# Kernel tuning notes

Hardware: AMD Instinct MI355X
Metric: run time of the kernel (lower is better)

Reference implementation:

```python
import jax, jax.numpy as jnp
import numpy as np

N = 50000
E = 800000
IN_DIM = 128
HID = 64
OUT_DIM = 128
NEG_SLOPE = 0.2  # PyG GATConv default


def _add_self_loops(src, dst, edge_attr, n):
    # PyG GATConv(add_self_loops=True) with edge_dim uses fill_value='mean':
    # self-loop edge_attr = mean of edge_attr of incoming edges per node.
    deg = jax.ops.segment_sum(jnp.ones((src.shape[0],), edge_attr.dtype), dst, num_segments=n)
    loop_attr = jax.ops.segment_sum(edge_attr, dst, num_segments=n) / jnp.maximum(deg, 1.0)[:, None]
    loop = jnp.arange(n, dtype=src.dtype)
    return (jnp.concatenate([src, loop]), jnp.concatenate([dst, loop]),
            jnp.concatenate([edge_attr, loop_attr], axis=0))


def _gat_conv(x, src, dst, edge_attr, W, We, a_src, a_dst, a_edge, bias, heads, out_dim, concat, n):
    src, dst, edge_attr = _add_self_loops(src, dst, edge_attr, n)
    h = (x @ W).reshape(n, heads, out_dim)                      # [N,H,D]
    he = (edge_attr @ We).reshape(-1, heads, out_dim)           # [E',H,D]
    alpha_src = jnp.einsum('nhd,hd->nh', h, a_src)
    alpha_dst = jnp.einsum('nhd,hd->nh', h, a_dst)
    alpha_edge = jnp.einsum('ehd,hd->eh', he, a_edge)
    alpha = jax.nn.leaky_relu(alpha_src[src] + alpha_dst[dst] + alpha_edge, NEG_SLOPE)  # [E',H]
    # segment softmax over edges grouped by destination node
    amax = jax.ops.segment_max(alpha, dst, num_segments=n)
    amax = jnp.where(jnp.isfinite(amax), amax, 0.0)
    ex = jnp.exp(alpha - amax[dst])
    denom = jax.ops.segment_sum(ex, dst, num_segments=n)
    coef = ex / (denom[dst] + 1e-16)                            # [E',H]
    msg = h[src] * coef[:, :, None]                             # [E',H,D]
    out = jax.ops.segment_sum(msg, dst, num_segments=n)         # [N,H,D]
    out = out.reshape(n, heads * out_dim) if concat else out.mean(axis=1)
    return out + bias


def setup_inputs() -> dict:
    key = jax.random.key(0)
    ks = jax.random.split(key, 16)
    s = 0.05
    inp = {
        'x': jax.random.normal(ks[0], (N, IN_DIM), jnp.float32),
        'edge_index': jax.random.randint(ks[1], (2, E), 0, N, dtype=jnp.int64),
        'edge_attr': jax.random.normal(ks[2], (E, 2), jnp.float32),
        # gat1: heads=4, concat -> out 4*HID
        'W1': jax.random.normal(ks[3], (IN_DIM, 4 * HID), jnp.float32) * s,
        'We1': jax.random.normal(ks[4], (2, 4 * HID), jnp.float32) * s,
        'asrc1': jax.random.normal(ks[5], (4, HID), jnp.float32) * s,
        'adst1': jax.random.normal(ks[6], (4, HID), jnp.float32) * s,
        'aedge1': jax.random.normal(ks[7], (4, HID), jnp.float32) * s,
        'b1': jnp.zeros((4 * HID,), jnp.float32),
        # gat2: heads=1, concat=False -> out OUT_DIM
        'W2': jax.random.normal(ks[8], (4 * HID, OUT_DIM), jnp.float32) * s,
        'We2': jax.random.normal(ks[9], (2, OUT_DIM), jnp.float32) * s,
        'asrc2': jax.random.normal(ks[10], (1, OUT_DIM), jnp.float32) * s,
        'adst2': jax.random.normal(ks[11], (1, OUT_DIM), jnp.float32) * s,
        'aedge2': jax.random.normal(ks[12], (1, OUT_DIM), jnp.float32) * s,
        'b2': jnp.zeros((OUT_DIM,), jnp.float32),
    }
    return inp


def reference(x, edge_index, edge_attr, W1, We1, asrc1, adst1, aedge1, b1,
              W2, We2, asrc2, adst2, aedge2, b2):
    src, dst = edge_index[0], edge_index[1]
    # dropout layers are identity in eval mode
    h = _gat_conv(x, src, dst, edge_attr, W1, We1, asrc1, adst1, aedge1, b1,
                  heads=4, out_dim=HID, concat=True, n=x.shape[0])
    h = jax.nn.elu(h)
    out = _gat_conv(h, src, dst, edge_attr, W2, We2, asrc2, adst2, aedge2, b2,
                    heads=1, out_dim=OUT_DIM, concat=False, n=x.shape[0])
    return out
```

## Files before the change

### kernel.cpp

```cpp
#include <hip/hip_runtime.h>
#include <hip/hip_bf16.h>

#define NN 50000
#define EE 800000
#define EP (EE + NN)
#define SCAN_B 2048
#define NB ((NN + SCAN_B - 1) / SCAN_B)


typedef short bf16x8 __attribute__((ext_vector_type(8)));
typedef float f32x4  __attribute__((ext_vector_type(4)));

__device__ __forceinline__ float bf2f(unsigned short u) {
    return __uint_as_float(((unsigned)u) << 16);
}
__device__ __forceinline__ unsigned short f2bf(float f) {
    unsigned b = __float_as_uint(f);
    b += 0x7fffu + ((b >> 16) & 1u);
    return (unsigned short)(b >> 16);
}

__global__ void k_prep(const float* __restrict__ We1, const float* __restrict__ ae1,
                       const float* __restrict__ We2, const float* __restrict__ ae2,
                       float* __restrict__ v,
                       const float* __restrict__ W1, unsigned short* __restrict__ W1t,
                       const float* __restrict__ W2, unsigned short* __restrict__ W2t,
                       const int* __restrict__ ei, int* __restrict__ idg,
                       const float* __restrict__ x, unsigned short* __restrict__ xb) {
    int bid = blockIdx.x, t = threadIdx.x;
    if (bid == 0) {
        if (t < 8) {
            int c = t >> 2, h = t & 3;
            float s = 0.f;
            for (int d = 0; d < 64; d++) s += We1[c * 256 + h * 64 + d] * ae1[h * 64 + d];
            v[c * 4 + h] = s;
        } else if (t < 10) {
            int c = t - 8;
            float s = 0.f;
            for (int d = 0; d < 128; d++) s += We2[c * 128 + d] * ae2[d];
            v[8 + c] = s;
        }
    } else if (bid <= 256) {
        int idx = (bid - 1) * 256 + t;
        if (idx < 32768) {
            int k = idx >> 8, n = idx & 255;
            W1t[n * 128 + k] = f2bf(W1[idx]);
        } else {
            int i = idx - 32768;
            int k = i >> 7, n = i & 127;
            W2t[n * 256 + k] = f2bf(W2[i]);
        }
    } else if (bid <= 256 + 3125) {
        int e = (bid - 257) * 256 + t;
        if (e < EE) atomicAdd(&idg[ei[EE + e]], 1);
    } else {
        int i = (bid - 3382) * 256 + t;
        if (i < NN * 128 / 4) {
            float4 vv = ((const float4*)x)[i];
            ushort4 o;
            o.x = f2bf(vv.x); o.y = f2bf(vv.y); o.z = f2bf(vv.z); o.w = f2bf(vv.w);
            ((ushort4*)xb)[i] = o;
        }
    }
}

__global__ void k_scan1(const int* __restrict__ idg, int* __restrict__ rowptr,
                        int* __restrict__ bsum) {
    __shared__ int sh[512];
    int t = threadIdx.x;
    int base = blockIdx.x * SCAN_B + t * 4;
    int v[4]; int s = 0;
    #pragma unroll
    for (int j = 0; j < 4; j++) {
        int i = base + j;
        v[j] = (i < NN) ? (idg[i] + 1) : 0;
        s += v[j];
    }
    sh[t] = s;
    __syncthreads();
    for (int off = 1; off < 512; off <<= 1) {
        int a = (t >= off) ? sh[t - off] : 0;
        __syncthreads();
        sh[t] += a;
        __syncthreads();
    }
    int run = sh[t] - s;
    #pragma unroll
    for (int j = 0; j < 4; j++) {
        int i = base + j;
        if (i < NN) rowptr[i] = run;
        run += v[j];
    }
    if (t == 511) bsum[blockIdx.x] = sh[511];
}

__global__ void k_scan2(const int* __restrict__ bsum, int* __restrict__ boff,
                        int* __restrict__ rowptr) {
    if (threadIdx.x == 0) {
        int acc = 0;
        for (int b = 0; b < NB; b++) { boff[b] = acc; acc += bsum[b]; }
        rowptr[NN] = acc;
    }
}

__global__ void k_scan3(int* __restrict__ rowptr, const int* __restrict__ boff) {
    int t = threadIdx.x;
    int i = blockIdx.x * SCAN_B + t * 4;
    int off = boff[blockIdx.x];
    #pragma unroll
    for (int j = 0; j < 4; j++)
        if (i + j < NN) rowptr[i + j] += off;
}

__global__ void k_scatter(const int* __restrict__ ei, const float* __restrict__ eattr,
                          const int* __restrict__ rowptr, int* __restrict__ cnt,
                          int2* __restrict__ slot) {
    int e = blockIdx.x * blockDim.x + threadIdx.x;
    if (e >= EE) return;
    int s = ei[e], d = ei[EE + e];
    int p = rowptr[d] + 1 + atomicAdd(&cnt[d], 1);
    unsigned a0 = f2bf(eattr[2 * e]), a1 = f2bf(eattr[2 * e + 1]);
    slot[p] = make_int2(s, (int)(a0 | (a1 << 16)));
}

__global__ void k_selfattr(const int* __restrict__ rowptr, int2* __restrict__ slot) {
    int n = blockIdx.x * blockDim.x + threadIdx.x;
    if (n >= NN) return;
    int beg = rowptr[n], end = rowptr[n + 1];
    float s0 = 0.f, s1 = 0.f;
    for (int p = beg + 1; p < end; p++) {
        unsigned a = (unsigned)slot[p].y;
        s0 += bf2f((unsigned short)(a & 0xffff));
        s1 += bf2f((unsigned short)(a >> 16));
    }
    float dg = fmaxf((float)(end - beg - 1), 1.0f);
    unsigned b0 = f2bf(s0 / dg), b1v = f2bf(s1 / dg);
    slot[beg] = make_int2(n, (int)(b0 | (b1v << 16)));
}

template <int K, int NT, int H>
__global__ __launch_bounds__(256) void gemm_mfma(const unsigned short* __restrict__ A,
                                                 const unsigned short* __restrict__ Bt,
                                                 unsigned short* __restrict__ C,
                                                 const float* __restrict__ avs,
                                                 const float* __restrict__ avd,
                                                 float* __restrict__ asrc,
                                                 float* __restrict__ adst,
                                                 int M, int N) {
    int wave = threadIdx.x >> 6, lane = threadIdx.x & 63;
    int l16 = lane & 15, quad = lane >> 4;
    int m0 = blockIdx.y * 128 + wave * 32;
    int n0 = blockIdx.x * (NT * 16);

    f32x4 acc[2][NT];
    #pragma unroll
    for (int mt = 0; mt < 2; mt++)
        #pragma unroll
        for (int nt = 0; nt < NT; nt++)
            acc[mt][nt] = (f32x4){0.f, 0.f, 0.f, 0.f};

    int ar0 = min(m0 + l16, M - 1);
    int ar1 = min(m0 + 16 + l16, M - 1);
    const unsigned short* a0 = A + (size_t)ar0 * K + quad * 8;
    const unsigned short* a1 = A + (size_t)ar1 * K + quad * 8;
    const unsigned short* bp = Bt + (size_t)(n0 + l16) * K + quad * 8;

    #pragma unroll
    for (int k0 = 0; k0 < K; k0 += 32) {
        bf16x8 af0 = *(const bf16x8*)(a0 + k0);
        bf16x8 af1 = *(const bf16x8*)(a1 + k0);
        #pragma unroll
        for (int nt = 0; nt < NT; nt++) {
            bf16x8 bf = *(const bf16x8*)(bp + (size_t)nt * 16 * K + k0);
            acc[0][nt] = __builtin_amdgcn_mfma_f32_16x16x32_bf16(af0, bf, acc[0][nt], 0, 0, 0);
            acc[1][nt] = __builtin_amdgcn_mfma_f32_16x16x32_bf16(af1, bf, acc[1][nt], 0, 0, 0);
        }
    }

    #pragma unroll
    for (int mt = 0; mt < 2; mt++)
        #pragma unroll
        for (int reg = 0; reg < 4; reg++) {
            int row = m0 + mt * 16 + quad * 4 + reg;
            if (row < M) {
                #pragma unroll
                for (int nt = 0; nt < NT; nt++)
                    C[(size_t)row * N + n0 + nt * 16 + l16] = f2bf(acc[mt][nt][reg]);
            }
        }

    float ws[NT], wd[NT];
    #pragma unroll
    for (int nt = 0; nt < NT; nt++) {
        ws[nt] = avs[n0 + nt * 16 + l16];
        wd[nt] = avd[n0 + nt * 16 + l16];
    }
    int hh = n0 >> 6;
    #pragma unroll
    for (int mt = 0; mt < 2; mt++)
        #pragma unroll
        for (int reg = 0; reg < 4; reg++) {
            int row = m0 + mt * 16 + quad * 4 + reg;
            float s1 = 0.f, s2 = 0.f;
            #pragma unroll
            for (int nt = 0; nt < NT; nt++) {
                float c = acc[mt][nt][reg];
                s1 += c * ws[nt];
                s2 += c * wd[nt];
            }
            #pragma unroll
            for (int off = 1; off < 16; off <<= 1) {
                s1 += __shfl_xor(s1, off);
                s2 += __shfl_xor(s2, off);
            }
            if (l16 == 0 && row < M) {
                asrc[row * H + hh] = s1;
                adst[row * H + hh] = s2;
            }
        }
}

__global__ __launch_bounds__(256) void k_agg1(const int* __restrict__ rowptr,
                       const int2* __restrict__ slot, const float* __restrict__ asrc,
                       const float* __restrict__ adst, const float* __restrict__ v,
                       const unsigned short* __restrict__ hb, const float* __restrict__ b1,
                       unsigned short* __restrict__ h2b) {
    int node = blockIdx.x * 4 + (threadIdx.x >> 6);
    if (node >= NN) return;
    int lane = threadIdx.x & 63;
    int j    = lane & 15;
    int hp   = lane >> 4;
    int half = lane >> 5;
    int hl   = lane & 31;
    int hh2  = hl >> 3;
    int beg = rowptr[node], end = rowptr[node + 1];
    float ad_p = adst[node * 4 + hp];
    float v0 = v[hp], v1 = v[4 + hp];
    float acc[8] = {};
    float den = 0.f;
    for (int pb = beg; pb < end; pb += 16) {
        int m = min(16, end - pb);
        int sj = 0; float exv = 0.f;
        if (j < m) {
            int2 sl = slot[pb + j];
            sj = sl.x;
            unsigned au = (unsigned)sl.y;
            float a0 = bf2f((unsigned short)(au & 0xffff));
            float a1 = bf2f((unsigned short)(au >> 16));
            float al = asrc[sj * 4 + hp] + ad_p + a0 * v0 + a1 * v1;
            al = (al > 0.f) ? al : 0.2f * al;
            exv = __expf(al);
        }
        den += exv;
        #pragma unroll 2
        for (int j2 = 0; j2 < m; j2 += 2) {
            int jj = j2 + half;
            int s   = __shfl(sj, jj);
            float w = __shfl(exv, jj + (hh2 << 4));
            bf16x8 raw = *(const bf16x8*)(hb + (size_t)s * 256 + hl * 8);
            #pragma unroll
            for (int k = 0; k < 8; k++)
                acc[k] += w * bf2f((unsigned short)raw[k]);
        }
    }
    #pragma unroll
    for (int k = 0; k < 8; k++)
        acc[k] += __shfl_down(acc[k], 32);
    #pragma unroll
    for (int off = 8; off; off >>= 1) den += __shfl_xor(den, off);
    float den_h = __shfl(den, hh2 << 4);
    if (lane < 32) {
        float inv = 1.f / (den_h + 1e-16f);
        short ov[8];
        #pragma unroll
        for (int k = 0; k < 8; k++) {
            float val = acc[k] * inv + b1[hl * 8 + k];
            val = (val > 0.f) ? val : __expf(val) - 1.f;
            ov[k] = (short)f2bf(val);
        }
        bf16x8 o = {ov[0], ov[1], ov[2], ov[3], ov[4], ov[5], ov[6], ov[7]};
        *(bf16x8*)(h2b + (size_t)node * 256 + hl * 8) = o;
    }
}

__global__ __launch_bounds__(256) void k_agg2(const int* __restrict__ rowptr,
                       const int2* __restrict__ slot, const float* __restrict__ asrc,
                       const float* __restrict__ adst, const float* __restrict__ v,
                       const unsigned short* __restrict__ gb, const float* __restrict__ b2,
                       float* __restrict__ outp) {
    int node = blockIdx.x * 4 + (threadIdx.x >> 6);
    if (node >= NN) return;
    int lane = threadIdx.x & 63;
    int q  = lane >> 4;
    int ql = lane & 15;
    int beg = rowptr[node], end = rowptr[node + 1];
    float ad = adst[node];
    float v0 = v[0], v1 = v[1];
    float acc[8] = {};
    float den = 0.f;
    for (int pb = beg; pb < end; pb += 64) {
        int m = min(64, end - pb);
        int sj = 0; float exv = 0.f;
        if (lane < m) {
            int2 sl = slot[pb + lane];
            sj = sl.x;
            unsigned au = (unsigned)sl.y;
            float a0 = bf2f((unsigned short)(au & 0xffff));
            float a1 = bf2f((unsigned short)(au >> 16));
            float al = asrc[sj] + ad + a0 * v0 + a1 * v1;
            al = (al > 0.f) ? al : 0.2f * al;
            exv = __expf(al);
        }
        den += exv;
        #pragma unroll 2
        for (int j2 = 0; j2 < m; j2 += 4) {
            int jj = j2 + q;
            int s   = __shfl(sj, jj);
            float w = __shfl(exv, jj);
            bf16x8 raw = *(const bf16x8*)(gb + (size_t)s * 128 + ql * 8);
            #pragma unroll
            for (int k = 0; k < 8; k++)
                acc[k] += w * bf2f((unsigned short)raw[k]);
        }
    }
    #pragma unroll
    for (int k = 0; k < 8; k++) {
        acc[k] += __shfl_down(acc[k], 32);
        acc[k] += __shfl_down(acc[k], 16);
    }
    #pragma unroll
    for (int off = 32; off; off >>= 1) den += __shfl_xor(den, off);
    if (lane < 16) {
        float inv = 1.f / (den + 1e-16f);
        float o[8];
        #pragma unroll
        for (int k = 0; k < 8; k++) o[k] = acc[k] * inv + b2[ql * 8 + k];
        float4 o0 = {o[0], o[1], o[2], o[3]};
        float4 o1 = {o[4], o[5], o[6], o[7]};
        *(float4*)(outp + (size_t)node * 128 + ql * 8)     = o0;
        *(float4*)(outp + (size_t)node * 128 + ql * 8 + 4) = o1;
    }
}

extern "C" void kernel_launch(void* const* d_in, const int* in_sizes, int n_in,
                              void* d_out, int out_size, void* d_ws, size_t ws_size,
                              hipStream_t stream) {
    const float* x     = (const float*)d_in[0];
    const int*   ei    = (const int*)d_in[1];
    const float* eattr = (const float*)d_in[2];
    const float* W1    = (const float*)d_in[3];
    const float* We1   = (const float*)d_in[4];
    const float* as1   = (const float*)d_in[5];
    const float* ad1   = (const float*)d_in[6];
    const float* ae1   = (const float*)d_in[7];
    const float* b1    = (const float*)d_in[8];
    const float* W2    = (const float*)d_in[9];
    const float* We2   = (const float*)d_in[10];
    const float* as2   = (const float*)d_in[11];
    const float* ad2   = (const float*)d_in[12];
    const float* ae2   = (const float*)d_in[13];
    const float* b2    = (const float*)d_in[14];
    float* out = (float*)d_out;

    int* idg    = (int*)d_ws;
    int* cnt    = idg + NN;
    int* rowptr = cnt + NN;
    int* bsum   = rowptr + NN + 16;
    int* boff   = bsum + 32;
    int2* slot  = (int2*)(boff + 32);
    float* asrc1 = (float*)(slot + EP);
    float* adst1 = asrc1 + 4 * NN;
    float* asrc2 = adst1 + 4 * NN;
    float* adst2 = asrc2 + NN;
    float* vbuf  = adst2 + NN;
    unsigned short* ub = (unsigned short*)(((uintptr_t)(vbuf + 64) + 63) & ~(uintptr_t)63);
    unsigned short* x_bf  = ub;
    unsigned short* W1t   = x_bf + (size_t)NN * 128;
    unsigned short* W2t   = W1t + 32768;
    unsigned short* h1_bf = W2t + 32768;
    unsigned short* h2_bf = h1_bf + (size_t)NN * 256;
    unsigned short* g2_bf = h2_bf + (size_t)NN * 256;

    hipMemsetAsync(idg, 0, (size_t)2 * NN * sizeof(int), stream);

    k_prep<<<9632, 256, 0, stream>>>(We1, ae1, We2, ae2, vbuf, W1, W1t, W2, W2t,
                                     ei, idg, x, x_bf);
    k_scan1<<<NB, 512, 0, stream>>>(idg, rowptr, bsum);
    k_scan2<<<1, 64, 0, stream>>>(bsum, boff, rowptr);
    k_scan3<<<NB, 512, 0, stream>>>(rowptr, boff);
    k_scatter<<<(EE + 255) / 256, 256, 0, stream>>>(ei, eattr, rowptr, cnt, slot);
    k_selfattr<<<(NN + 255) / 256, 256, 0, stream>>>(rowptr, slot);

    gemm_mfma<128, 4, 4><<<dim3(4, (NN + 127) / 128), 256, 0, stream>>>(
        x_bf, W1t, h1_bf, as1, ad1, asrc1, adst1, NN, 256);
    k_agg1<<<(NN + 3) / 4, 256, 0, stream>>>(rowptr, slot, asrc1, adst1, vbuf,
                                             h1_bf, b1, h2_bf);

    gemm_mfma<256, 8, 1><<<dim3(1, (NN + 127) / 128), 256, 0, stream>>>(
        h2_bf, W2t, g2_bf, as2, ad2, asrc2, adst2, NN, 128);
    k_agg2<<<(NN + 3) / 4, 256, 0, stream>>>(rowptr, slot, asrc2, adst2, vbuf + 8,
                                             g2_bf, b2, out);
}
```

Before: 353.9 us.

## Fuse scan into single block and compute self-loop attrs via atomics

```diff
diff --git a/kernel.cpp b/kernel.cpp
--- a/kernel.cpp
+++ b/kernel.cpp
@@ -4,8 +4,6 @@
 #define NN 50000
 #define EE 800000
 #define EP (EE + NN)
-#define SCAN_B 2048
-#define NB ((NN + SCAN_B - 1) / SCAN_B)
 
 
 typedef short bf16x8 __attribute__((ext_vector_type(8)));
@@ -18,6 +16,9 @@
     unsigned b = __float_as_uint(f);
     b += 0x7fffu + ((b >> 16) & 1u);
     return (unsigned short)(b >> 16);
+}
+__device__ __forceinline__ float2 bfpair(unsigned u) {
+    return make_float2(__uint_as_float(u << 16), __uint_as_float(u & 0xffff0000u));
 }
 
 __global__ void k_prep(const float* __restrict__ We1, const float* __restrict__ ae1,
@@ -25,7 +26,8 @@
                        float* __restrict__ v,
                        const float* __restrict__ W1, unsigned short* __restrict__ W1t,
                        const float* __restrict__ W2, unsigned short* __restrict__ W2t,
-                       const int* __restrict__ ei, int* __restrict__ idg,
+                       const int* __restrict__ ei, const float* __restrict__ eattr,
+                       int* __restrict__ idg, float* __restrict__ lsum,
                        const float* __restrict__ x, unsigned short* __restrict__ xb) {
     int bid = blockIdx.x, t = threadIdx.x;
     if (bid == 0) {
@@ -52,7 +54,13 @@
         }
     } else if (bid <= 256 + 3125) {
         int e = (bid - 257) * 256 + t;
-        if (e < EE) atomicAdd(&idg[ei[EE + e]], 1);
+        if (e < EE) {
+            int d = ei[EE + e];
+            float2 a = ((const float2*)eattr)[e];
+            atomicAdd(&idg[d], 1);
+            atomicAdd(&lsum[2 * d],     a.x);
+            atomicAdd(&lsum[2 * d + 1], a.y);
+        }
     } else {
         int i = (bid - 3382) * 256 + t;
         if (i < NN * 128 / 4) {
@@ -64,78 +72,57 @@
     }
 }
 
-__global__ void k_scan1(const int* __restrict__ idg, int* __restrict__ rowptr,
-                        int* __restrict__ bsum) {
-    __shared__ int sh[512];
+#define CHUNK 49
+__global__ __launch_bounds__(1024) void k_scan(const int* __restrict__ idg,
+                                               int* __restrict__ rowptr) {
+    __shared__ int sh[1024];
     int t = threadIdx.x;
-    int base = blockIdx.x * SCAN_B + t * 4;
-    int v[4]; int s = 0;
-    #pragma unroll
-    for (int j = 0; j < 4; j++) {
+    int base = t * CHUNK;
+    int loc[CHUNK];
+    int s = 0;
+    #pragma unroll
+    for (int j = 0; j < CHUNK; j++) {
         int i = base + j;
-        v[j] = (i < NN) ? (idg[i] + 1) : 0;
-        s += v[j];
+        loc[j] = s;
+        s += (i < NN) ? (idg[i] + 1) : 0;
     }
     sh[t] = s;
     __syncthreads();
-    for (int off = 1; off < 512; off <<= 1) {
+    for (int off = 1; off < 1024; off <<= 1) {
         int a = (t >= off) ? sh[t - off] : 0;
         __syncthreads();
         sh[t] += a;
         __syncthreads();
     }
-    int run = sh[t] - s;
-    #pragma unroll
-    for (int j = 0; j < 4; j++) {
+    int pre = sh[t] - s;
+    #pragma unroll
+    for (int j = 0; j < CHUNK; j++) {
         int i = base + j;
-        if (i < NN) rowptr[i] = run;
-        run += v[j];
-    }
-    if (t == 511) bsum[blockIdx.x] = sh[511];
-}
-
-__global__ void k_scan2(const int* __restrict__ bsum, int* __restrict__ boff,
-                        int* __restrict__ rowptr) {
-    if (threadIdx.x == 0) {
-        int acc = 0;
-        for (int b = 0; b < NB; b++) { boff[b] = acc; acc += bsum[b]; }
-        rowptr[NN] = acc;
-    }
-}
-
-__global__ void k_scan3(int* __restrict__ rowptr, const int* __restrict__ boff) {
-    int t = threadIdx.x;
-    int i = blockIdx.x * SCAN_B + t * 4;
-    int off = boff[blockIdx.x];
-    #pragma unroll
-    for (int j = 0; j < 4; j++)
-        if (i + j < NN) rowptr[i + j] += off;
+        if (i < NN) rowptr[i] = pre + loc[j];
+    }
+    if (t == 1023) rowptr[NN] = sh[1023];
 }
 
 __global__ void k_scatter(const int* __restrict__ ei, const float* __restrict__ eattr,
                           const int* __restrict__ rowptr, int* __restrict__ cnt,
+                          const int* __restrict__ idg, const float* __restrict__ lsum,
                           int2* __restrict__ slot) {
-    int e = blockIdx.x * blockDim.x + threadIdx.x;
-    if (e >= EE) return;
-    int s = ei[e], d = ei[EE + e];
-    int p = rowptr[d] + 1 + atomicAdd(&cnt[d], 1);
-    unsigned a0 = f2bf(eattr[2 * e]), a1 = f2bf(eattr[2 * e + 1]);
-    slot[p] = make_int2(s, (int)(a0 | (a1 << 16)));
-}
-
-__global__ void k_selfattr(const int* __restrict__ rowptr, int2* __restrict__ slot) {
-    int n = blockIdx.x * blockDim.x + threadIdx.x;
-    if (n >= NN) return;
-    int beg = rowptr[n], end = rowptr[n + 1];
-    float s0 = 0.f, s1 = 0.f;
-    for (int p = beg + 1; p < end; p++) {
-        unsigned a = (unsigned)slot[p].y;
-        s0 += bf2f((unsigned short)(a & 0xffff));
-        s1 += bf2f((unsigned short)(a >> 16));
-    }
-    float dg = fmaxf((float)(end - beg - 1), 1.0f);
-    unsigned b0 = f2bf(s0 / dg), b1v = f2bf(s1 / dg);
-    slot[beg] = make_int2(n, (int)(b0 | (b1v << 16)));
+    int bid = blockIdx.x, t = threadIdx.x;
+    if (bid < 3125) {
+        int e = bid * 256 + t;
+        if (e >= EE) return;
+        int s = ei[e], d = ei[EE + e];
+        int p = rowptr[d] + 1 + atomicAdd(&cnt[d], 1);
+        float2 a = ((const float2*)eattr)[e];
+        unsigned a0 = f2bf(a.x), a1 = f2bf(a.y);
+        slot[p] = make_int2(s, (int)(a0 | (a1 << 16)));
+    } else {
+        int n = (bid - 3125) * 256 + t;
+        if (n >= NN) return;
+        float dg = fmaxf((float)idg[n], 1.0f);
+        unsigned b0 = f2bf(lsum[2 * n] / dg), b1v = f2bf(lsum[2 * n + 1] / dg);
+        slot[rowptr[n]] = make_int2(n, (int)(b0 | (b1v << 16)));
+    }
 }
 
 template <int K, int NT, int H>
@@ -236,7 +223,7 @@
     int beg = rowptr[node], end = rowptr[node + 1];
     float ad_p = adst[node * 4 + hp];
     float v0 = v[hp], v1 = v[4 + hp];
-    float acc[8] = {};
+    float2 acc2[4] = {};
     float den = 0.f;
     for (int pb = beg; pb < end; pb += 16) {
         int m = min(16, end - pb);
@@ -245,9 +232,8 @@
             int2 sl = slot[pb + j];
             sj = sl.x;
             unsigned au = (unsigned)sl.y;
-            float a0 = bf2f((unsigned short)(au & 0xffff));
-            float a1 = bf2f((unsigned short)(au >> 16));
-            float al = asrc[sj * 4 + hp] + ad_p + a0 * v0 + a1 * v1;
+            float2 a = bfpair(au);
+            float al = asrc[sj * 4 + hp] + ad_p + a.x * v0 + a.y * v1;
             al = (al > 0.f) ? al : 0.2f * al;
             exv = __expf(al);
         }
@@ -257,15 +243,20 @@
             int jj = j2 + half;
             int s   = __shfl(sj, jj);
             float w = __shfl(exv, jj + (hh2 << 4));
-            bf16x8 raw = *(const bf16x8*)(hb + (size_t)s * 256 + hl * 8);
-            #pragma unroll
-            for (int k = 0; k < 8; k++)
-                acc[k] += w * bf2f((unsigned short)raw[k]);
-        }
-    }
-    #pragma unroll
-    for (int k = 0; k < 8; k++)
-        acc[k] += __shfl_down(acc[k], 32);
+            uint4 raw = *(const uint4*)(hb + (size_t)s * 256 + hl * 8);
+            float2 p0 = bfpair(raw.x), p1 = bfpair(raw.y);
+            float2 p2 = bfpair(raw.z), p3 = bfpair(raw.w);
+            acc2[0].x += w * p0.x; acc2[0].y += w * p0.y;
+            acc2[1].x += w * p1.x; acc2[1].y += w * p1.y;
+            acc2[2].x += w * p2.x; acc2[2].y += w * p2.y;
+            acc2[3].x += w * p3.x; acc2[3].y += w * p3.y;
+        }
+    }
+    #pragma unroll
+    for (int k = 0; k < 4; k++) {
+        acc2[k].x += __shfl_down(acc2[k].x, 32);
+        acc2[k].y += __shfl_down(acc2[k].y, 32);
+    }
     #pragma unroll
     for (int off = 8; off; off >>= 1) den += __shfl_xor(den, off);
     float den_h = __shfl(den, hh2 << 4);
@@ -273,10 +264,13 @@
         float inv = 1.f / (den_h + 1e-16f);
         short ov[8];
         #pragma unroll
-        for (int k = 0; k < 8; k++) {
-            float val = acc[k] * inv + b1[hl * 8 + k];
-            val = (val > 0.f) ? val : __expf(val) - 1.f;
-            ov[k] = (short)f2bf(val);
+        for (int k = 0; k < 4; k++) {
+            float va = acc2[k].x * inv + b1[hl * 8 + 2 * k];
+            float vb = acc2[k].y * inv + b1[hl * 8 + 2 * k + 1];
+            va = (va > 0.f) ? va : __expf(va) - 1.f;
+            vb = (vb > 0.f) ? vb : __expf(vb) - 1.f;
+            ov[2 * k]     = (short)f2bf(va);
+            ov[2 * k + 1] = (short)f2bf(vb);
         }
         bf16x8 o = {ov[0], ov[1], ov[2], ov[3], ov[4], ov[5], ov[6], ov[7]};
         *(bf16x8*)(h2b + (size_t)node * 256 + hl * 8) = o;
@@ -296,7 +290,7 @@
     int beg = rowptr[node], end = rowptr[node + 1];
     float ad = adst[node];
     float v0 = v[0], v1 = v[1];
-    float acc[8] = {};
+    float2 acc2[4] = {};
     float den = 0.f;
     for (int pb = beg; pb < end; pb += 64) {
         int m = min(64, end - pb);
@@ -304,10 +298,8 @@
         if (lane < m) {
             int2 sl = slot[pb + lane];
             sj = sl.x;
-            unsigned au = (unsigned)sl.y;
-            float a0 = bf2f((unsigned short)(au & 0xffff));
-            float a1 = bf2f((unsigned short)(au >> 16));
-            float al = asrc[sj] + ad + a0 * v0 + a1 * v1;
+            float2 a = bfpair((unsigned)sl.y);
+            float al = asrc[sj] + ad + a.x * v0 + a.y * v1;
             al = (al > 0.f) ? al : 0.2f * al;
             exv = __expf(al);
         }
@@ -317,26 +309,35 @@
             int jj = j2 + q;
             int s   = __shfl(sj, jj);
             float w = __shfl(exv, jj);
-            bf16x8 raw = *(const bf16x8*)(gb + (size_t)s * 128 + ql * 8);
-            #pragma unroll
-            for (int k = 0; k < 8; k++)
-                acc[k] += w * bf2f((unsigned short)raw[k]);
-        }
-    }
-    #pragma unroll
-    for (int k = 0; k < 8; k++) {
-        acc[k] += __shfl_down(acc[k], 32);
-        acc[k] += __shfl_down(acc[k], 16);
+            uint4 raw = *(const uint4*)(gb + (size_t)s * 128 + ql * 8);
+            float2 p0 = bfpair(raw.x), p1 = bfpair(raw.y);
+            float2 p2 = bfpair(raw.z), p3 = bfpair(raw.w);
+            acc2[0].x += w * p0.x; acc2[0].y += w * p0.y;
+            acc2[1].x += w * p1.x; acc2[1].y += w * p1.y;
+            acc2[2].x += w * p2.x; acc2[2].y += w * p2.y;
+            acc2[3].x += w * p3.x; acc2[3].y += w * p3.y;
+        }
+    }
+    #pragma unroll
+    for (int k = 0; k < 4; k++) {
+        acc2[k].x += __shfl_down(acc2[k].x, 32);
+        acc2[k].y += __shfl_down(acc2[k].y, 32);
+        acc2[k].x += __shfl_down(acc2[k].x, 16);
+        acc2[k].y += __shfl_down(acc2[k].y, 16);
     }
     #pragma unroll
     for (int off = 32; off; off >>= 1) den += __shfl_xor(den, off);
     if (lane < 16) {
         float inv = 1.f / (den + 1e-16f);
-        float o[8];
-        #pragma unroll
-        for (int k = 0; k < 8; k++) o[k] = acc[k] * inv + b2[ql * 8 + k];
-        float4 o0 = {o[0], o[1], o[2], o[3]};
-        float4 o1 = {o[4], o[5], o[6], o[7]};
+        float4 o0, o1;
+        o0.x = acc2[0].x * inv + b2[ql * 8 + 0];
+        o0.y = acc2[0].y * inv + b2[ql * 8 + 1];
+        o0.z = acc2[1].x * inv + b2[ql * 8 + 2];
+        o0.w = acc2[1].y * inv + b2[ql * 8 + 3];
+        o1.x = acc2[2].x * inv + b2[ql * 8 + 4];
+        o1.y = acc2[2].y * inv + b2[ql * 8 + 5];
+        o1.z = acc2[3].x * inv + b2[ql * 8 + 6];
+        o1.w = acc2[3].y * inv + b2[ql * 8 + 7];
         *(float4*)(outp + (size_t)node * 128 + ql * 8)     = o0;
         *(float4*)(outp + (size_t)node * 128 + ql * 8 + 4) = o1;
     }
@@ -364,10 +365,9 @@
 
     int* idg    = (int*)d_ws;
     int* cnt    = idg + NN;
-    int* rowptr = cnt + NN;
-    int* bsum   = rowptr + NN + 16;
-    int* boff   = bsum + 32;
-    int2* slot  = (int2*)(boff + 32);
+    float* lsum = (float*)(cnt + NN);
+    int* rowptr = (int*)(lsum + 2 * NN);
+    int2* slot  = (int2*)(rowptr + NN + 16);
     float* asrc1 = (float*)(slot + EP);
     float* adst1 = asrc1 + 4 * NN;
     float* asrc2 = adst1 + 4 * NN;
@@ -381,15 +381,13 @@
     unsigned short* h2_bf = h1_bf + (size_t)NN * 256;
     unsigned short* g2_bf = h2_bf + (size_t)NN * 256;
 
-    hipMemsetAsync(idg, 0, (size_t)2 * NN * sizeof(int), stream);
+    hipMemsetAsync(idg, 0, (size_t)4 * NN * sizeof(int), stream);
 
     k_prep<<<9632, 256, 0, stream>>>(We1, ae1, We2, ae2, vbuf, W1, W1t, W2, W2t,
-                                     ei, idg, x, x_bf);
-    k_scan1<<<NB, 512, 0, stream>>>(idg, rowptr, bsum);
-    k_scan2<<<1, 64, 0, stream>>>(bsum, boff, rowptr);
-    k_scan3<<<NB, 512, 0, stream>>>(rowptr, boff);
-    k_scatter<<<(EE + 255) / 256, 256, 0, stream>>>(ei, eattr, rowptr, cnt, slot);
-    k_selfattr<<<(NN + 255) / 256, 256, 0, stream>>>(rowptr, slot);
+                                     ei, eattr, idg, lsum, x, x_bf);
+    k_scan<<<1, 1024, 0, stream>>>(idg, rowptr);
+    k_scatter<<<3125 + (NN + 255) / 256, 256, 0, stream>>>(ei, eattr, rowptr, cnt,
+                                                           idg, lsum, slot);
 
     gemm_mfma<128, 4, 4><<<dim3(4, (NN + 127) / 128), 256, 0, stream>>>(
         x_bf, W1t, h1_bf, as1, ad1, asrc1, adst1, NN, 256);
```

New measurement: 469.7 us. +32.7%, slower.
